# Performance work log

Hardware: AMD Instinct MI355X
Metric: run time of the kernel (lower is better)

The kernel has to match this reference:

```python
import jax, jax.numpy as jnp
import numpy as np


def _diag_scale_grid_sample(x, scale_factors):
    """Equivalent of F.affine_grid(diag(s) affine, align_corners=False) followed by
    F.grid_sample(x, grid, mode='bilinear', padding_mode='zeros', align_corners=False).
    Because the affine is diagonal with zero translation, the grid is separable in
    x and y, so we do two 1D bilinear interpolations instead of a full 2D gather.
    x: [B, C, H, W] float; scale_factors: [2] (sx, sy)."""
    B, C, H, W = x.shape
    sx, sy = scale_factors[0], scale_factors[1]

    # affine_grid normalized output coords (align_corners=False): (2k+1)/N - 1
    xs = (2.0 * jnp.arange(W, dtype=x.dtype) + 1.0) / W - 1.0  # [W]
    ys = (2.0 * jnp.arange(H, dtype=x.dtype) + 1.0) / H - 1.0  # [H]
    gx = sx * xs  # normalized sample x coords, [W]
    gy = sy * ys  # normalized sample y coords, [H]

    # grid_sample unnormalize (align_corners=False): ((g+1)*N - 1)/2
    ix = ((gx + 1.0) * W - 1.0) * 0.5  # [W] input pixel x coords
    iy = ((gy + 1.0) * H - 1.0) * 0.5  # [H] input pixel y coords

    ix0f = jnp.floor(ix)
    iy0f = jnp.floor(iy)
    wx1 = ix - ix0f  # weight for right neighbor
    wy1 = iy - iy0f  # weight for bottom neighbor
    wx0 = 1.0 - wx1
    wy0 = 1.0 - wy1

    ix0 = ix0f.astype(jnp.int32)
    ix1 = ix0 + 1
    iy0 = iy0f.astype(jnp.int32)
    iy1 = iy0 + 1

    # zeros padding: out-of-bounds corners contribute 0
    vx0 = ((ix0 >= 0) & (ix0 < W)).astype(x.dtype)
    vx1 = ((ix1 >= 0) & (ix1 < W)).astype(x.dtype)
    vy0 = ((iy0 >= 0) & (iy0 < H)).astype(x.dtype)
    vy1 = ((iy1 >= 0) & (iy1 < H)).astype(x.dtype)

    ix0c = jnp.clip(ix0, 0, W - 1)
    ix1c = jnp.clip(ix1, 0, W - 1)
    iy0c = jnp.clip(iy0, 0, H - 1)
    iy1c = jnp.clip(iy1, 0, H - 1)

    # interpolate along H: [B, C, H_out, W]
    xh = (x[:, :, iy0c, :] * (wy0 * vy0)[None, None, :, None]
          + x[:, :, iy1c, :] * (wy1 * vy1)[None, None, :, None])
    # interpolate along W: [B, C, H_out, W_out]
    out = (xh[:, :, :, ix0c] * (wx0 * vx0)[None, None, None, :]
           + xh[:, :, :, ix1c] * (wx1 * vx1)[None, None, None, :])
    return out


def setup_inputs() -> dict:
    key = jax.random.key(0)
    k1, _ = jax.random.split(key)
    x = jax.random.normal(k1, (32, 3, 512, 512), dtype=jnp.float32)
    scale_factors = jnp.ones((2,), dtype=jnp.float32)
    return {"x": x, "scale_factors": scale_factors}


def reference(x, scale_factors):
    return _diag_scale_grid_sample(x, scale_factors)
```

## Files before the change

### kernel.cpp

```cpp
#include <hip/hip_runtime.h>

#define BD 32
#define CD 3
#define HD 512
#define WD 512

__global__ __launch_bounds__(256) void stn_kernel(const float* __restrict__ x,
                                                  const float* __restrict__ sf,
                                                  float* __restrict__ out) {
    __shared__ float xh[WD];

    const int plane = blockIdx.x;
    const int h     = blockIdx.y;
    const float sx = sf[0];
    const float sy = sf[1];

    float ysn  = (2.0f * (float)h + 1.0f) / (float)HD - 1.0f;
    float iy   = ((sy * ysn + 1.0f) * (float)HD - 1.0f) * 0.5f;
    float iy0f = floorf(iy);
    float wy1  = iy - iy0f;
    int   iy0  = (int)iy0f;
    int   iy1  = iy0 + 1;
    float fy0  = (iy0 >= 0 && iy0 < HD) ? (1.0f - wy1) : 0.0f;
    float fy1  = (iy1 >= 0 && iy1 < HD) ? wy1 : 0.0f;
    int   iy0c = min(max(iy0, 0), HD - 1);
    int   iy1c = min(max(iy1, 0), HD - 1);

    const float* row0 = x + ((long long)plane * HD + iy0c) * WD;
    const float* row1 = x + ((long long)plane * HD + iy1c) * WD;

    const int t = threadIdx.x;

    float2 a = ((const float2*)row0)[t];
    float2 b = ((const float2*)row1)[t];
    float2 c;
    c.x = a.x * fy0 + b.x * fy1;
    c.y = a.y * fy0 + b.y * fy1;
    ((float2*)xh)[t] = c;
    __syncthreads();

    float2 o;
#pragma unroll
    for (int j = 0; j < 2; ++j) {
        int   w    = 2 * t + j;
        float xsn  = (2.0f * (float)w + 1.0f) / (float)WD - 1.0f;
        float ix   = ((sx * xsn + 1.0f) * (float)WD - 1.0f) * 0.5f;
        float ix0f = floorf(ix);
        float wx1  = ix - ix0f;
        int   ix0  = (int)ix0f;
        int   ix1  = ix0 + 1;
        float fx0  = (ix0 >= 0 && ix0 < WD) ? (1.0f - wx1) : 0.0f;
        float fx1  = (ix1 >= 0 && ix1 < WD) ? wx1 : 0.0f;
        int   ix0c = min(max(ix0, 0), WD - 1);
        int   ix1c = min(max(ix1, 0), WD - 1);
        ((float*)&o)[j] = xh[ix0c] * fx0 + xh[ix1c] * fx1;
    }

    ((float2*)(out + ((long long)plane * HD + h) * WD))[t] = o;
}

extern "C" void kernel_launch(void* const* d_in, const int* in_sizes, int n_in,
                              void* d_out, int out_size, void* d_ws, size_t ws_size,
                              hipStream_t stream) {
    const float* x  = (const float*)d_in[0];
    const float* sf = (const float*)d_in[1];
    float* out      = (float*)d_out;

    dim3 grid(BD * CD, HD);
    stn_kernel<<<grid, 256, 0, stream>>>(x, sf, out);
}
```

Measured before the change: 186.8 us.

## Process eight output rows per block with float4 loads

Each block now handles a tile of 8 output rows instead of one, loading both source rows for each with float4 vector loads into a 2D shared buffer. The x-interpolation indices and weights are computed once per block and reused across the rows. This cuts block count and per-block launch/sync overhead and raises memory-level parallelism. In exchange it uses more registers and shared memory and gives fewer blocks in the grid.

```diff
diff --git a/kernel.cpp b/kernel.cpp
--- a/kernel.cpp
+++ b/kernel.cpp
@@ -4,42 +4,56 @@
 #define CD 3
 #define HD 512
 #define WD 512
+#define TH 8
 
 __global__ __launch_bounds__(256) void stn_kernel(const float* __restrict__ x,
                                                   const float* __restrict__ sf,
                                                   float* __restrict__ out) {
-    __shared__ float xh[WD];
+    __shared__ float xh[TH][WD];
 
     const int plane = blockIdx.x;
-    const int h     = blockIdx.y;
+    const int h0    = blockIdx.y * TH;
     const float sx = sf[0];
     const float sy = sf[1];
 
-    float ysn  = (2.0f * (float)h + 1.0f) / (float)HD - 1.0f;
-    float iy   = ((sy * ysn + 1.0f) * (float)HD - 1.0f) * 0.5f;
-    float iy0f = floorf(iy);
-    float wy1  = iy - iy0f;
-    int   iy0  = (int)iy0f;
-    int   iy1  = iy0 + 1;
-    float fy0  = (iy0 >= 0 && iy0 < HD) ? (1.0f - wy1) : 0.0f;
-    float fy1  = (iy1 >= 0 && iy1 < HD) ? wy1 : 0.0f;
-    int   iy0c = min(max(iy0, 0), HD - 1);
-    int   iy1c = min(max(iy1, 0), HD - 1);
+    const int t  = threadIdx.x;
+    const int rr = t >> 7;
+    const int c4 = (t & 127) << 2;
 
-    const float* row0 = x + ((long long)plane * HD + iy0c) * WD;
-    const float* row1 = x + ((long long)plane * HD + iy1c) * WD;
+    const float* xp = x + (long long)plane * HD * WD;
 
-    const int t = threadIdx.x;
-
-    float2 a = ((const float2*)row0)[t];
-    float2 b = ((const float2*)row1)[t];
-    float2 c;
-    c.x = a.x * fy0 + b.x * fy1;
-    c.y = a.y * fy0 + b.y * fy1;
-    ((float2*)xh)[t] = c;
+    float4 A[4], B[4];
+    float  fy0v[4], fy1v[4];
+#pragma unroll
+    for (int rp = 0; rp < 4; ++rp) {
+        int   h    = h0 + rp * 2 + rr;
+        float ysn  = (2.0f * (float)h + 1.0f) / (float)HD - 1.0f;
+        float iy   = ((sy * ysn + 1.0f) * (float)HD - 1.0f) * 0.5f;
+        float iy0f = floorf(iy);
+        float wy1  = iy - iy0f;
+        int   iy0  = (int)iy0f;
+        int   iy1  = iy0 + 1;
+        fy0v[rp]   = (iy0 >= 0 && iy0 < HD) ? (1.0f - wy1) : 0.0f;
+        fy1v[rp]   = (iy1 >= 0 && iy1 < HD) ? wy1 : 0.0f;
+        int iy0c   = min(max(iy0, 0), HD - 1);
+        int iy1c   = min(max(iy1, 0), HD - 1);
+        A[rp] = *(const float4*)(xp + (long long)iy0c * WD + c4);
+        B[rp] = *(const float4*)(xp + (long long)iy1c * WD + c4);
+    }
+#pragma unroll
+    for (int rp = 0; rp < 4; ++rp) {
+        int    r = rp * 2 + rr;
+        float4 c;
+        c.x = A[rp].x * fy0v[rp] + B[rp].x * fy1v[rp];
+        c.y = A[rp].y * fy0v[rp] + B[rp].y * fy1v[rp];
+        c.z = A[rp].z * fy0v[rp] + B[rp].z * fy1v[rp];
+        c.w = A[rp].w * fy0v[rp] + B[rp].w * fy1v[rp];
+        *(float4*)&xh[r][c4] = c;
+    }
     __syncthreads();
 
-    float2 o;
+    int   ix0c[2], ix1c[2];
+    float fx0[2], fx1[2];
 #pragma unroll
     for (int j = 0; j < 2; ++j) {
         int   w    = 2 * t + j;
@@ -49,14 +63,20 @@
         float wx1  = ix - ix0f;
         int   ix0  = (int)ix0f;
         int   ix1  = ix0 + 1;
-        float fx0  = (ix0 >= 0 && ix0 < WD) ? (1.0f - wx1) : 0.0f;
-        float fx1  = (ix1 >= 0 && ix1 < WD) ? wx1 : 0.0f;
-        int   ix0c = min(max(ix0, 0), WD - 1);
-        int   ix1c = min(max(ix1, 0), WD - 1);
-        ((float*)&o)[j] = xh[ix0c] * fx0 + xh[ix1c] * fx1;
+        fx0[j]     = (ix0 >= 0 && ix0 < WD) ? (1.0f - wx1) : 0.0f;
+        fx1[j]     = (ix1 >= 0 && ix1 < WD) ? wx1 : 0.0f;
+        ix0c[j]    = min(max(ix0, 0), WD - 1);
+        ix1c[j]    = min(max(ix1, 0), WD - 1);
     }
 
-    ((float2*)(out + ((long long)plane * HD + h) * WD))[t] = o;
+    float* outp = out + ((long long)plane * HD + h0) * WD;
+#pragma unroll
+    for (int r = 0; r < TH; ++r) {
+        float2 o;
+        o.x = xh[r][ix0c[0]] * fx0[0] + xh[r][ix1c[0]] * fx1[0];
+        o.y = xh[r][ix0c[1]] * fx0[1] + xh[r][ix1c[1]] * fx1[1];
+        ((float2*)(outp + (long long)r * WD))[t] = o;
+    }
 }
 
 extern "C" void kernel_launch(void* const* d_in, const int* in_sizes, int n_in,
@@ -66,6 +86,6 @@
     const float* sf = (const float*)d_in[1];
     float* out      = (float*)d_out;
 
-    dim3 grid(BD * CD, HD);
+    dim3 grid(BD * CD, HD / TH);
     stn_kernel<<<grid, 256, 0, stream>>>(x, sf, out);
 }
```

After: 179.7 us. 3.8% less time.

## Process 8 output rows per block using direct global-to-LDS loads

Applied to the files above, without the earlier changes.

Each block now handles 8 output rows instead of one, so the grid is 8x smaller. For each row it loads both source rows straight into shared memory with global_load_lds, 16 bytes per lane. Vertical interpolation is deferred to the read-out phase, and the horizontal weights are folded into a clamped base index pair. This targets per-block launch overhead and register-staged copies, at the cost of 32KB of shared memory per block, which may lower occupancy and adds redundant row reads.

```diff
diff --git a/kernel.cpp b/kernel.cpp
--- a/kernel.cpp
+++ b/kernel.cpp
@@ -4,42 +4,51 @@
 #define CD 3
 #define HD 512
 #define WD 512
+#define TH 8
+#define NSLOT (2 * TH)
+
+typedef __attribute__((address_space(1))) const void GV;
+typedef __attribute__((address_space(3))) void LV;
 
 __global__ __launch_bounds__(256) void stn_kernel(const float* __restrict__ x,
                                                   const float* __restrict__ sf,
                                                   float* __restrict__ out) {
-    __shared__ float xh[WD];
+    __shared__ float xh[NSLOT][WD];
 
     const int plane = blockIdx.x;
-    const int h     = blockIdx.y;
+    const int h0    = blockIdx.y * TH;
     const float sx = sf[0];
     const float sy = sf[1];
 
-    float ysn  = (2.0f * (float)h + 1.0f) / (float)HD - 1.0f;
-    float iy   = ((sy * ysn + 1.0f) * (float)HD - 1.0f) * 0.5f;
-    float iy0f = floorf(iy);
-    float wy1  = iy - iy0f;
-    int   iy0  = (int)iy0f;
-    int   iy1  = iy0 + 1;
-    float fy0  = (iy0 >= 0 && iy0 < HD) ? (1.0f - wy1) : 0.0f;
-    float fy1  = (iy1 >= 0 && iy1 < HD) ? wy1 : 0.0f;
-    int   iy0c = min(max(iy0, 0), HD - 1);
-    int   iy1c = min(max(iy1, 0), HD - 1);
+    const int t = threadIdx.x;
+    const int p = t >> 7;
+    const int l = t & 127;
 
-    const float* row0 = x + ((long long)plane * HD + iy0c) * WD;
-    const float* row1 = x + ((long long)plane * HD + iy1c) * WD;
+    const float* xp = x + (long long)plane * HD * WD;
 
-    const int t = threadIdx.x;
-
-    float2 a = ((const float2*)row0)[t];
-    float2 b = ((const float2*)row1)[t];
-    float2 c;
-    c.x = a.x * fy0 + b.x * fy1;
-    c.y = a.y * fy0 + b.y * fy1;
-    ((float2*)xh)[t] = c;
+    float fy0[TH], fy1[TH];
+#pragma unroll
+    for (int s = 0; s < TH; ++s) {
+        int   h    = h0 + s;
+        float ysn  = (2.0f * (float)h + 1.0f) / (float)HD - 1.0f;
+        float iy   = ((sy * ysn + 1.0f) * (float)HD - 1.0f) * 0.5f;
+        float iy0f = floorf(iy);
+        float wy1  = iy - iy0f;
+        int   iy0  = (int)iy0f;
+        int   iy1  = iy0 + 1;
+        fy0[s] = (iy0 >= 0 && iy0 < HD) ? (1.0f - wy1) : 0.0f;
+        fy1[s] = (iy1 >= 0 && iy1 < HD) ? wy1 : 0.0f;
+        int iy0c = min(max(iy0, 0), HD - 1);
+        int iy1c = min(max(iy1, 0), HD - 1);
+        int rowc = p ? iy1c : iy0c;
+        const float* src = xp + (long long)rowc * WD + (l << 2);
+        __builtin_amdgcn_global_load_lds((GV*)src, (LV*)&xh[2 * s + p][l << 2],
+                                         16, 0, 0);
+    }
     __syncthreads();
 
-    float2 o;
+    float wa[2], wb[2];
+    int   basec[2];
 #pragma unroll
     for (int j = 0; j < 2; ++j) {
         int   w    = 2 * t + j;
@@ -51,12 +60,29 @@
         int   ix1  = ix0 + 1;
         float fx0  = (ix0 >= 0 && ix0 < WD) ? (1.0f - wx1) : 0.0f;
         float fx1  = (ix1 >= 0 && ix1 < WD) ? wx1 : 0.0f;
-        int   ix0c = min(max(ix0, 0), WD - 1);
-        int   ix1c = min(max(ix1, 0), WD - 1);
-        ((float*)&o)[j] = xh[ix0c] * fx0 + xh[ix1c] * fx1;
+        int   base = min(max(ix0, 0), WD - 2);
+        basec[j] = base;
+        wa[j] = (ix0 == base) ? fx0 : ((ix1 == base) ? fx1 : 0.0f);
+        wb[j] = (ix0 == base + 1) ? fx0 : ((ix1 == base + 1) ? fx1 : 0.0f);
     }
 
-    ((float2*)(out + ((long long)plane * HD + h) * WD))[t] = o;
+    float* outp = out + ((long long)plane * HD + h0) * WD + 2 * t;
+#pragma unroll
+    for (int r = 0; r < TH; ++r) {
+        float2 o;
+#pragma unroll
+        for (int j = 0; j < 2; ++j) {
+            int   b   = basec[j];
+            float v0  = xh[2 * r][b];
+            float v1  = xh[2 * r][b + 1];
+            float u0  = xh[2 * r + 1][b];
+            float u1  = xh[2 * r + 1][b + 1];
+            float hv0 = v0 * fy0[r] + u0 * fy1[r];
+            float hv1 = v1 * fy0[r] + u1 * fy1[r];
+            ((float*)&o)[j] = hv0 * wa[j] + hv1 * wb[j];
+        }
+        *(float2*)(outp + (long long)r * WD) = o;
+    }
 }
 
 extern "C" void kernel_launch(void* const* d_in, const int* in_sizes, int n_in,
@@ -66,6 +92,6 @@
     const float* sf = (const float*)d_in[1];
     float* out      = (float*)d_out;
 
-    dim3 grid(BD * CD, HD);
+    dim3 grid(BD * CD, HD / TH);
     stn_kernel<<<grid, 256, 0, stream>>>(x, sf, out);
 }
```

Result: faster. 182.1 us (-2.5%).
